# Performance work log

Measured on AMD Instinct MI355X. Metric: run time of the kernel, lower is better.

## Reference

```python
import jax, jax.numpy as jnp
import numpy as np

EMBED_DIM = 256
NUM_HEADS = 8
HEAD_DIM = EMBED_DIM // NUM_HEADS
SPARSITY_RATIO = 0.1
NEG_INF = float('-inf')


def setup_inputs() -> dict:
    key = jax.random.key(0)
    ks = jax.random.split(key, 6)
    B, S, E = 4, 2048, EMBED_DIM
    scale = 1.0 / np.sqrt(E)
    x = jax.random.normal(ks[0], (B, S, E), dtype=jnp.float32)
    Wq = jax.random.normal(ks[1], (E, E), dtype=jnp.float32) * scale
    Wk = jax.random.normal(ks[2], (E, E), dtype=jnp.float32) * scale
    Wv = jax.random.normal(ks[3], (E, E), dtype=jnp.float32) * scale
    Wo = jax.random.normal(ks[4], (E, E), dtype=jnp.float32) * scale
    z = jnp.zeros((E,), dtype=jnp.float32)
    return {"x": x, "Wq": Wq, "bq": z, "Wk": Wk, "bk": z,
            "Wv": Wv, "bv": z, "Wo": Wo, "bo": z}


def _sparse_mask(x):
    # no_grad block in torch -> stop_gradient here
    B, S, E = x.shape
    scores = jnp.einsum('bse,bte->bst', x, x) / np.sqrt(EMBED_DIM)  # [B,S,S]
    k = max(1, int(S * SPARSITY_RATIO))
    _, idx = jax.lax.top_k(scores, k)  # [B,S,k]
    sparse = jnp.zeros_like(scores)
    bi = jnp.arange(B)[:, None, None]
    si = jnp.arange(S)[None, :, None]
    sparse = sparse.at[bi, si, idx].set(1.0)
    attn_mask = jnp.where(sparse > 0, 0.0, NEG_INF).astype(x.dtype)  # [B,S,S]
    return jax.lax.stop_gradient(attn_mask)


def reference(x, Wq, bq, Wk, bk, Wv, bv, Wo, bo):
    B, S, E = x.shape
    H, D = NUM_HEADS, HEAD_DIM
    attn_mask = _sparse_mask(x)  # [B,S,S], additive 0/-inf

    q = (x @ Wq.T + bq).reshape(B, S, H, D)
    k = (x @ Wk.T + bk).reshape(B, S, H, D)
    v = (x @ Wv.T + bv).reshape(B, S, H, D)

    logits = jnp.einsum('bshd,bthd->bhst', q, k) / np.sqrt(D)  # [B,H,S,S]
    logits = logits + attn_mask[:, None, :, :]
    probs = jax.nn.softmax(logits, axis=-1)  # dropout is identity in eval

    ctx = jnp.einsum('bhst,bthd->bshd', probs, v).reshape(B, S, E)
    out = ctx @ Wo.T + bo
    attn_weights = probs.mean(axis=1)  # averaged over heads [B,S,S]
    return out, attn_weights
```

## Files before the change

kernel.cpp:

```cpp
#include <hip/hip_runtime.h>

#define SEQ  2048
#define EMB  256
#define NH   8
#define HD   32
#define NB   4
#define KTOP 204
#define IDXP 208
#define KPW  52
#define MBOUND 4e-4f

typedef unsigned long long ull;
typedef unsigned short u16;

using frag8  = __attribute__((ext_vector_type(8))) short;
using f32x4v = __attribute__((ext_vector_type(4))) float;
typedef _Float16 f16;
typedef _Float16 f16x2 __attribute__((ext_vector_type(2)));

union U4 { uint4 u; f16x2 h[4]; };
union HU { f16 h; u16 u; };

#if defined(__has_builtin)
#if __has_builtin(__builtin_amdgcn_fdot2)
#define FDOT2(a,b,c) __builtin_amdgcn_fdot2(a, b, c, false)
#endif
#endif
#ifndef FDOT2
__device__ __forceinline__ float fdot2_sw(f16x2 a, f16x2 b, float c) {
  return c + (float)a[0]*(float)b[0] + (float)a[1]*(float)b[1];
}
#define FDOT2(a,b,c) fdot2_sw(a,b,c)
#endif

__device__ __forceinline__ unsigned f2ord(float f) {
  unsigned u = __float_as_uint(f);
  return (u & 0x80000000u) ? ~u : (u | 0x80000000u);
}
__device__ __forceinline__ float ord2f(unsigned o) {
  unsigned u = (o & 0x80000000u) ? (o ^ 0x80000000u) : ~o;
  return __uint_as_float(u);
}
__device__ __forceinline__ u16 f2bf(float f) {
  unsigned u = __float_as_uint(f);
  u += 0x7FFF + ((u >> 16) & 1);
  return (u16)(u >> 16);
}
__device__ __forceinline__ float bf2f(u16 h) {
  return __uint_as_float((unsigned)h << 16);
}

__device__ __forceinline__ void tk_radix(
    const unsigned key[8], int tid, int (*hist)[256], int* sel,
    unsigned& V, int& MEQ)
{
  const int lane = tid & 63, wid = tid >> 6;
  unsigned prefix = 0;
  int k = KTOP;
#pragma unroll
  for (int p = 0; p < 4; ++p) {
    const int shift = 24 - 8 * p;
    hist[0][tid] = 0; hist[1][tid] = 0; hist[2][tid] = 0; hist[3][tid] = 0;
    __syncthreads();
#pragma unroll
    for (int j = 0; j < 8; ++j) {
      unsigned kj = key[j];
      bool ok = (p == 0) || ((kj >> (shift + 8)) == prefix);
      if (ok) atomicAdd(&hist[wid][(kj >> shift) & 255], 1);
    }
    __syncthreads();
    {
      int c = hist[0][tid] + hist[1][tid] + hist[2][tid] + hist[3][tid];
      hist[0][tid] = c;
    }
    __syncthreads();
    if (wid == 0) {
      int m0 = hist[0][lane * 4 + 0], m1 = hist[0][lane * 4 + 1];
      int m2 = hist[0][lane * 4 + 2], m3 = hist[0][lane * 4 + 3];
      int sl = m0 + m1 + m2 + m3;
      int suf = sl;
#pragma unroll
      for (int off = 1; off < 64; off <<= 1) {
        int y = __shfl_down(suf, off, 64);
        if (lane + off < 64) suf += y;
      }
      int above = suf - sl;
      if (above < k && k <= suf) {
        int bin, nk;
        if (k <= above + m3)                { bin = lane*4+3; nk = k - above; }
        else if (k <= above + m3 + m2)      { bin = lane*4+2; nk = k - above - m3; }
        else if (k <= above + m3 + m2 + m1) { bin = lane*4+1; nk = k - above - m3 - m2; }
        else                                { bin = lane*4+0; nk = k - above - m3 - m2 - m1; }
        sel[0] = bin; sel[1] = nk;
      }
    }
    __syncthreads();
    prefix = (prefix << 8) | (unsigned)sel[0];
    k = sel[1];
    __syncthreads();
  }
  V = prefix;
  MEQ = k;
}

__device__ __forceinline__ int tk_scan_excl(int v, int tid, int* wsum) {
  const int lane = tid & 63, wid = tid >> 6;
  int x = v;
#pragma unroll
  for (int off = 1; off < 64; off <<= 1) {
    int y = __shfl_up(x, off, 64);
    if (lane >= off) x += y;
  }
  if (lane == 63) wsum[wid] = x;
  __syncthreads();
  int base = 0;
  for (int w = 0; w < wid; ++w) base += wsum[w];
  return base + x - v;
}

__device__ __forceinline__ void tk_write(const unsigned key[8], unsigned V, int MEQ,
                                         int tid, u16* orow, int* wsum) {
  int ceq = 0;
#pragma unroll
  for (int j = 0; j < 8; ++j) ceq += (key[j] == V) ? 1 : 0;
  int run = tk_scan_excl(ceq, tid, wsum);
  unsigned bits = 0;
#pragma unroll
  for (int j = 0; j < 8; ++j) {
    bool e = (key[j] == V);
    bool s = (key[j] > V) || (e && (run < MEQ));
    if (e) run++;
    if (s) bits |= (1u << j);
  }
  int csel = __popc(bits);
  __syncthreads();
  int base = tk_scan_excl(csel, tid, wsum);
#pragma unroll
  for (int j = 0; j < 8; ++j)
    if ((bits >> j) & 1u) orow[base++] = (u16)(tid * 8 + j);
}

__global__ __launch_bounds__(256) void pack_x(
    const float* __restrict__ x, u16* __restrict__ xh, u16* __restrict__ xl,
    int* __restrict__ flagcnt)
{
  if (flagcnt && blockIdx.x == 0 && threadIdx.x < NB) flagcnt[threadIdx.x] = 0;
  const int i = (blockIdx.x * 256 + threadIdx.x) * 8;
  float4 a = *(const float4*)(x + i);
  float4 b = *(const float4*)(x + i + 4);
  float v[8] = {a.x,a.y,a.z,a.w,b.x,b.y,b.z,b.w};
  u16 h[8], l[8];
#pragma unroll
  for (int j = 0; j < 8; ++j) {
    h[j] = f2bf(v[j]);
    l[j] = f2bf(v[j] - bf2f(h[j]));
  }
  uint4 ph, pl;
  ph.x = h[0] | ((unsigned)h[1] << 16); ph.y = h[2] | ((unsigned)h[3] << 16);
  ph.z = h[4] | ((unsigned)h[5] << 16); ph.w = h[6] | ((unsigned)h[7] << 16);
  pl.x = l[0] | ((unsigned)l[1] << 16); pl.y = l[2] | ((unsigned)l[3] << 16);
  pl.z = l[4] | ((unsigned)l[5] << 16); pl.w = l[6] | ((unsigned)l[7] << 16);
  *(uint4*)(xh + i) = ph;
  *(uint4*)(xl + i) = pl;
}

__global__ __launch_bounds__(256) void pack_w(
    const float* __restrict__ W0, const float* __restrict__ W1,
    const float* __restrict__ W2, const float* __restrict__ W3,
    u16* __restrict__ wpk)
{
  const int m = blockIdx.y;
  const float* W = (m == 0) ? W0 : (m == 1) ? W1 : (m == 2) ? W2 : W3;
  const int i = (blockIdx.x * 256 + threadIdx.x) * 8;
  float4 a = *(const float4*)(W + i);
  float4 b = *(const float4*)(W + i + 4);
  float v[8] = {a.x,a.y,a.z,a.w,b.x,b.y,b.z,b.w};
  u16 h[8], l[8];
#pragma unroll
  for (int j = 0; j < 8; ++j) {
    h[j] = f2bf(v[j]);
    l[j] = f2bf(v[j] - bf2f(h[j]));
  }
  uint4 ph, pl;
  ph.x = h[0] | ((unsigned)h[1] << 16); ph.y = h[2] | ((unsigned)h[3] << 16);
  ph.z = h[4] | ((unsigned)h[5] << 16); ph.w = h[6] | ((unsigned)h[7] << 16);
  pl.x = l[0] | ((unsigned)l[1] << 16); pl.y = l[2] | ((unsigned)l[3] << 16);
  pl.z = l[4] | ((unsigned)l[5] << 16); pl.w = l[6] | ((unsigned)l[7] << 16);
  u16* dh = wpk + (size_t)m * 2 * 65536;
  *(uint4*)(dh + i) = ph;
  *(uint4*)(dh + 65536 + i) = pl;
}

__global__ __launch_bounds__(256) void scores_mfma(
    const u16* __restrict__ xh, const u16* __restrict__ xl,
    float* __restrict__ C)
{
  __shared__ u16 Ah[128 * 40], Al[128 * 40], Bh[128 * 40], Bl[128 * 40];
  const int tid = threadIdx.x;
  const int m0 = blockIdx.x * 128, n0 = blockIdx.y * 128;
  const u16* xhB = xh + (size_t)blockIdx.z * SEQ * EMB;
  const u16* xlB = xl + (size_t)blockIdx.z * SEQ * EMB;
  float* Cb = C + (size_t)blockIdx.z * SEQ * SEQ;
  const int wv = tid >> 6, ln = tid & 63;
  const int quad = ln >> 4, r16 = ln & 15;
  const int wm = (wv & 1) * 64, wn = (wv >> 1) * 64;
  const int srow = tid >> 1, shalf = (tid & 1) * 16;

  f32x4v acc[4][4];
#pragma unroll
  for (int i = 0; i < 4; ++i)
#pragma unroll
    for (int j = 0; j < 4; ++j) acc[i][j] = (f32x4v){0.f, 0.f, 0.f, 0.f};

  for (int k0 = 0; k0 < EMB; k0 += 32) {
    __syncthreads();
    {
      size_t ga = (size_t)(m0 + srow) * EMB + k0 + shalf;
      size_t gb = (size_t)(n0 + srow) * EMB + k0 + shalf;
      uint4 ah0 = *(const uint4*)(xhB + ga), ah1 = *(const uint4*)(xhB + ga + 8);
      uint4 al0 = *(const uint4*)(xlB + ga), al1 = *(const uint4*)(xlB + ga + 8);
      uint4 bh0 = *(const uint4*)(xhB + gb), bh1 = *(const uint4*)(xhB + gb + 8);
      uint4 bl0 = *(const uint4*)(xlB + gb), bl1 = *(const uint4*)(xlB + gb + 8);
      int o = srow * 40 + shalf;
      *(uint4*)&Ah[o] = ah0; *(uint4*)&Ah[o + 8] = ah1;
      *(uint4*)&Al[o] = al0; *(uint4*)&Al[o + 8] = al1;
      *(uint4*)&Bh[o] = bh0; *(uint4*)&Bh[o + 8] = bh1;
      *(uint4*)&Bl[o] = bl0; *(uint4*)&Bl[o + 8] = bl1;
    }
    __syncthreads();
    frag8 fbh[4], fbl[4];
#pragma unroll
    for (int nt = 0; nt < 4; ++nt) {
      int ob = (wn + nt * 16 + r16) * 40 + quad * 8;
      fbh[nt] = *(const frag8*)&Bh[ob];
      fbl[nt] = *(const frag8*)&Bl[ob];
    }
#pragma unroll
    for (int mt = 0; mt < 4; ++mt) {
      int oa = (wm + mt * 16 + r16) * 40 + quad * 8;
      frag8 fah = *(const frag8*)&Ah[oa];
      frag8 fal = *(const frag8*)&Al[oa];
#pragma unroll
      for (int nt = 0; nt < 4; ++nt) {
        acc[mt][nt] = __builtin_amdgcn_mfma_f32_16x16x32_bf16(fah, fbh[nt], acc[mt][nt], 0, 0, 0);
        acc[mt][nt] = __builtin_amdgcn_mfma_f32_16x16x32_bf16(fah, fbl[nt], acc[mt][nt], 0, 0, 0);
        acc[mt][nt] = __builtin_amdgcn_mfma_f32_16x16x32_bf16(fal, fbh[nt], acc[mt][nt], 0, 0, 0);
        acc[mt][nt] = __builtin_amdgcn_mfma_f32_16x16x32_bf16(fal, fbl[nt], acc[mt][nt], 0, 0, 0);
      }
    }
  }
#pragma unroll
  for (int mt = 0; mt < 4; ++mt)
#pragma unroll
    for (int nt = 0; nt < 4; ++nt) {
      int cg = n0 + wn + nt * 16 + r16;
      int rb = m0 + wm + mt * 16 + quad * 4;
#pragma unroll
      for (int r = 0; r < 4; ++r)
        Cb[(size_t)(rb + r) * SEQ + cg] = acc[mt][nt][r] * 0.0625f;
    }
}

__global__ __launch_bounds__(256) void qkv_mfma(
    const u16* __restrict__ xh, const u16* __restrict__ xl,
    const u16* __restrict__ wpk,
    const float* __restrict__ bq, const float* __restrict__ bk,
    const float* __restrict__ bv,
    u16* __restrict__ qo, u16* __restrict__ ko, u16* __restrict__ vo)
{
  const int z = blockIdx.z;
  const u16* Wh = wpk + (size_t)z * 2 * 65536;
  const u16* Wl = Wh + 65536;
  const float* bias = (z == 0) ? bq : (z == 1) ? bk : bv;
  u16* out = (z == 0) ? qo : (z == 1) ? ko : vo;

  __shared__ u16 Ah[128 * 40], Al[128 * 40], Bh[128 * 40], Bl[128 * 40];
  const int tid = threadIdx.x;
  const int m0 = blockIdx.x * 128, n0 = blockIdx.y * 128;
  const int wv = tid >> 6, ln = tid & 63;
  const int quad = ln >> 4, r16 = ln & 15;
  const int wm = (wv & 1) * 64, wn = (wv >> 1) * 64;
  const int srow = tid >> 1, shalf = (tid & 1) * 16;

  f32x4v acc[4][4];
#pragma unroll
  for (int i = 0; i < 4; ++i)
#pragma unroll
    for (int j = 0; j < 4; ++j) acc[i][j] = (f32x4v){0.f, 0.f, 0.f, 0.f};

  for (int k0 = 0; k0 < EMB; k0 += 32) {
    __syncthreads();
    {
      size_t ga = (size_t)(m0 + srow) * EMB + k0 + shalf;
      size_t gb = (size_t)(n0 + srow) * EMB + k0 + shalf;
      uint4 ah0 = *(const uint4*)(xh + ga), ah1 = *(const uint4*)(xh + ga + 8);
      uint4 al0 = *(const uint4*)(xl + ga), al1 = *(const uint4*)(xl + ga + 8);
      uint4 bh0 = *(const uint4*)(Wh + gb), bh1 = *(const uint4*)(Wh + gb + 8);
      uint4 bl0 = *(const uint4*)(Wl + gb), bl1 = *(const uint4*)(Wl + gb + 8);
      int o = srow * 40 + shalf;
      *(uint4*)&Ah[o] = ah0; *(uint4*)&Ah[o + 8] = ah1;
      *(uint4*)&Al[o] = al0; *(uint4*)&Al[o + 8] = al1;
      *(uint4*)&Bh[o] = bh0; *(uint4*)&Bh[o + 8] = bh1;
      *(uint4*)&Bl[o] = bl0; *(uint4*)&Bl[o + 8] = bl1;
    }
    __syncthreads();
    frag8 fbh[4], fbl[4];
#pragma unroll
    for (int nt = 0; nt < 4; ++nt) {
      int ob = (wn + nt * 16 + r16) * 40 + quad * 8;
      fbh[nt] = *(const frag8*)&Bh[ob];
      fbl[nt] = *(const frag8*)&Bl[ob];
    }
#pragma unroll
    for (int mt = 0; mt < 4; ++mt) {
      int oa = (wm + mt * 16 + r16) * 40 + quad * 8;
      frag8 fah = *(const frag8*)&Ah[oa];
      frag8 fal = *(const frag8*)&Al[oa];
#pragma unroll
      for (int nt = 0; nt < 4; ++nt) {
        acc[mt][nt] = __builtin_amdgcn_mfma_f32_16x16x32_bf16(fah, fbh[nt], acc[mt][nt], 0, 0, 0);
        acc[mt][nt] = __builtin_amdgcn_mfma_f32_16x16x32_bf16(fah, fbl[nt], acc[mt][nt], 0, 0, 0);
        acc[mt][nt] = __builtin_amdgcn_mfma_f32_16x16x32_bf16(fal, fbh[nt], acc[mt][nt], 0, 0, 0);
      }
    }
  }
#pragma unroll
  for (int nt = 0; nt < 4; ++nt) {
    int cg = n0 + wn + nt * 16 + r16;
    float bvv = bias[cg];
#pragma unroll
    for (int mt = 0; mt < 4; ++mt) {
      int rb = m0 + wm + mt * 16 + quad * 4;
#pragma unroll
      for (int r = 0; r < 4; ++r) {
        HU hu; hu.h = (f16)(acc[mt][nt][r] + bvv);
        out[(size_t)(rb + r) * EMB + cg] = hu.u;
      }
    }
  }
}

__global__ __launch_bounds__(256) void out_mfma(
    const u16* __restrict__ ch, const u16* __restrict__ cl,
    const u16* __restrict__ wpk, const float* __restrict__ bias,
    float* __restrict__ out)
{
  const u16* Wh = wpk + (size_t)3 * 2 * 65536;
  const u16* Wl = Wh + 65536;
  __shared__ u16 Ah[128 * 40], Al[128 * 40], Bh[128 * 40], Bl[128 * 40];
  const int tid = threadIdx.x;
  const int m0 = blockIdx.x * 128, n0 = blockIdx.y * 128;
  const int wv = tid >> 6, ln = tid & 63;
  const int quad = ln >> 4, r16 = ln & 15;
  const int wm = (wv & 1) * 64, wn = (wv >> 1) * 64;
  const int srow = tid >> 1, shalf = (tid & 1) * 16;

  f32x4v acc[4][4];
#pragma unroll
  for (int i = 0; i < 4; ++i)
#pragma unroll
    for (int j = 0; j < 4; ++j) acc[i][j] = (f32x4v){0.f, 0.f, 0.f, 0.f};

  for (int k0 = 0; k0 < EMB; k0 += 32) {
    __syncthreads();
    {
      size_t ga = (size_t)(m0 + srow) * EMB + k0 + shalf;
      size_t gb = (size_t)(n0 + srow) * EMB + k0 + shalf;
      uint4 ah0 = *(const uint4*)(ch + ga), ah1 = *(const uint4*)(ch + ga + 8);
      uint4 al0 = *(const uint4*)(cl + ga), al1 = *(const uint4*)(cl + ga + 8);
      uint4 bh0 = *(const uint4*)(Wh + gb), bh1 = *(const uint4*)(Wh + gb + 8);
      uint4 bl0 = *(const uint4*)(Wl + gb), bl1 = *(const uint4*)(Wl + gb + 8);
      int o = srow * 40 + shalf;
      *(uint4*)&Ah[o] = ah0; *(uint4*)&Ah[o + 8] = ah1;
      *(uint4*)&Al[o] = al0; *(uint4*)&Al[o + 8] = al1;
      *(uint4*)&Bh[o] = bh0; *(uint4*)&Bh[o + 8] = bh1;
      *(uint4*)&Bl[o] = bl0; *(uint4*)&Bl[o + 8] = bl1;
    }
    __syncthreads();
    frag8 fbh[4], fbl[4];
#pragma unroll
    for (int nt = 0; nt < 4; ++nt) {
      int ob = (wn + nt * 16 + r16) * 40 + quad * 8;
      fbh[nt] = *(const frag8*)&Bh[ob];
      fbl[nt] = *(const frag8*)&Bl[ob];
    }
#pragma unroll
    for (int mt = 0; mt < 4; ++mt) {
      int oa = (wm + mt * 16 + r16) * 40 + quad * 8;
      frag8 fah = *(const frag8*)&Ah[oa];
      frag8 fal = *(const frag8*)&Al[oa];
#pragma unroll
      for (int nt = 0; nt < 4; ++nt) {
        acc[mt][nt] = __builtin_amdgcn_mfma_f32_16x16x32_bf16(fah, fbh[nt], acc[mt][nt], 0, 0, 0);
        acc[mt][nt] = __builtin_amdgcn_mfma_f32_16x16x32_bf16(fah, fbl[nt], acc[mt][nt], 0, 0, 0);
        acc[mt][nt] = __builtin_amdgcn_mfma_f32_16x16x32_bf16(fal, fbh[nt], acc[mt][nt], 0, 0, 0);
      }
    }
  }
#pragma unroll
  for (int nt = 0; nt < 4; ++nt) {
    int cg = n0 + wn + nt * 16 + r16;
    float bvv = bias[cg];
#pragma unroll
    for (int mt = 0; mt < 4; ++mt) {
      int rb = m0 + wm + mt * 16 + quad * 4;
#pragma unroll
      for (int r = 0; r < 4; ++r)
        out[(size_t)(rb + r) * EMB + cg] = acc[mt][nt][r] + bvv;
    }
  }
}

__global__ __launch_bounds__(256) void topk_idx(
    const float* __restrict__ scores, u16* __restrict__ idxl,
    int* __restrict__ flagcnt, int* __restrict__ flaglist)
{
  __shared__ int hist[4][256];
  __shared__ int sel[2];
  __shared__ int wsum[4];
  __shared__ unsigned wmax[4];
  const int r = blockIdx.x;
  const int tid = threadIdx.x;
  const int lane = tid & 63, wid = tid >> 6;
  const float* row = scores + (size_t)r * SEQ;
  unsigned key[8];
  {
    float4 f0 = *(const float4*)(row + tid * 8);
    float4 f1 = *(const float4*)(row + tid * 8 + 4);
    key[0]=f2ord(f0.x); key[1]=f2ord(f0.y); key[2]=f2ord(f0.z); key[3]=f2ord(f0.w);
    key[4]=f2ord(f1.x); key[5]=f2ord(f1.y); key[6]=f2ord(f1.z); key[7]=f2ord(f1.w);
  }
  unsigned V; int MEQ;
  tk_radix(key, tid, hist, sel, V, MEQ);

  {
    int ceq = 0; unsigned mk = 0;
#pragma unroll
    for (int j = 0; j < 8; ++j) {
      ceq += (key[j] == V) ? 1 : 0;
      if (key[j] < V && key[j] > mk) mk = key[j];
    }
#pragma unroll
    for (int off = 32; off > 0; off >>= 1) {
      ceq += __shfl_down(ceq, off, 64);
      unsigned o = (unsigned)__shfl_down((int)mk, off, 64);
      if (o > mk) mk = o;
    }
    if (lane == 0) { wsum[wid] = ceq; wmax[wid] = mk; }
    __syncthreads();
    if (tid == 0) {
      int EQ = wsum[0] + wsum[1] + wsum[2] + wsum[3];
      unsigned m2 = wmax[0];
      for (int w = 1; w < 4; ++w) if (wmax[w] > m2) m2 = wmax[w];
      bool flag = (EQ > MEQ) || !(ord2f(V) - ord2f(m2) >= MBOUND);
      if (flag) {
        int bb = r >> 11;
        int p = atomicAdd(&flagcnt[bb], 1);
        flaglist[bb * SEQ + p] = r & (SEQ - 1);
      }
    }
    __syncthreads();
  }

  tk_write(key, V, MEQ, tid, idxl + (size_t)r * IDXP, wsum);
}

__global__ __launch_bounds__(256) void fixup_gemm(
    const float* __restrict__ x, const int* __restrict__ flagcnt,
    const int* __restrict__ flaglist, float* __restrict__ attn)
{
  const int b = blockIdx.z;
  const int n = flagcnt[b];
  const int g0 = blockIdx.y * 64;
  if (g0 >= n) return;
  __shared__ float As[16][68];
  __shared__ float Bs[16][68];
  __shared__ int rowsh[64];
  const int tid = threadIdx.x;
  const int n0 = blockIdx.x * 64;
  if (tid < 64) {
    int gi = g0 + tid;
    rowsh[tid] = (gi < n) ? flaglist[b * SEQ + gi] : -1;
  }
  __syncthreads();
  const float* xb = x + (size_t)b * SEQ * EMB;
  const int lm = tid >> 2;
  const int lk = (tid & 3) << 2;
  const int mt = tid >> 4;
  const int nt = tid & 15;
  const int arow = rowsh[lm];
  const int arowL = (arow < 0) ? 0 : arow;
  float acc[4][4] = {{0.f}};
  for (int k0 = 0; k0 < EMB; k0 += 16) {
    float4 av = *(const float4*)(xb + (size_t)arowL * EMB + k0 + lk);
    float4 bv = *(const float4*)(xb + (size_t)(n0 + lm) * EMB + k0 + lk);
    __syncthreads();
    As[lk+0][lm] = av.x; As[lk+1][lm] = av.y; As[lk+2][lm] = av.z; As[lk+3][lm] = av.w;
    Bs[lk+0][lm] = bv.x; Bs[lk+1][lm] = bv.y; Bs[lk+2][lm] = bv.z; Bs[lk+3][lm] = bv.w;
    __syncthreads();
#pragma unroll
    for (int kk = 0; kk < 16; ++kk) {
      float4 a4 = *(const float4*)&As[kk][mt << 2];
      float4 b4 = *(const float4*)&Bs[kk][nt << 2];
      acc[0][0] += a4.x*b4.x; acc[0][1] += a4.x*b4.y; acc[0][2] += a4.x*b4.z; acc[0][3] += a4.x*b4.w;
      acc[1][0] += a4.y*b4.x; acc[1][1] += a4.y*b4.y; acc[1][2] += a4.y*b4.z; acc[1][3] += a4.y*b4.w;
      acc[2][0] += a4.z*b4.x; acc[2][1] += a4.z*b4.y; acc[2][2] += a4.z*b4.z; acc[2][3] += a4.z*b4.w;
      acc[3][0] += a4.w*b4.x; acc[3][1] += a4.w*b4.y; acc[3][2] += a4.w*b4.z; acc[3][3] += a4.w*b4.w;
    }
  }
  float* attnB = attn + (size_t)b * SEQ * SEQ;
#pragma unroll
  for (int r = 0; r < 4; ++r) {
    int rr = rowsh[(mt << 2) + r];
    if (rr >= 0) {
      float4 o;
      o.x = acc[r][0] * 0.0625f; o.y = acc[r][1] * 0.0625f;
      o.z = acc[r][2] * 0.0625f; o.w = acc[r][3] * 0.0625f;
      *(float4*)(attnB + (size_t)rr * SEQ + n0 + (nt << 2)) = o;
    }
  }
}

__global__ __launch_bounds__(256) void topk_fixup(
    const float* __restrict__ attn, const int* __restrict__ flagcnt,
    const int* __restrict__ flaglist, u16* __restrict__ idxl)
{
  const int b = blockIdx.y;
  if ((int)blockIdx.x >= flagcnt[b]) return;
  const int r = b * SEQ + flaglist[b * SEQ + blockIdx.x];
  __shared__ int hist[4][256];
  __shared__ int sel[2];
  __shared__ int wsum[4];
  const int tid = threadIdx.x;
  const float* row = attn + (size_t)r * SEQ;
  unsigned key[8];
  {
    float4 f0 = *(const float4*)(row + tid * 8);
    float4 f1 = *(const float4*)(row + tid * 8 + 4);
    key[0]=f2ord(f0.x); key[1]=f2ord(f0.y); key[2]=f2ord(f0.z); key[3]=f2ord(f0.w);
    key[4]=f2ord(f1.x); key[5]=f2ord(f1.y); key[6]=f2ord(f1.z); key[7]=f2ord(f1.w);
  }
  unsigned V; int MEQ;
  tk_radix(key, tid, hist, sel, V, MEQ);
  tk_write(key, V, MEQ, tid, idxl + (size_t)r * IDXP, wsum);
}

__global__ __launch_bounds__(256) void sparse_attn(
    const u16* __restrict__ qf, const u16* __restrict__ kf,
    const u16* __restrict__ vf, const u16* __restrict__ idxl,
    float* __restrict__ attn, float* __restrict__ ctxb)
{
  const int lin = blockIdx.x;
  const int b = lin & 3;
  const int q = (lin >> 3) + (((lin >> 2) & 1) << 10);
  const int tid = threadIdx.x;
  const int wv = tid >> 6, ln = tid & 63;
  const int half = ln >> 5, sl = ln & 31;
  const int h = sl >> 2, d0 = sl * 8;
  const int lb = sl * 16;
  __shared__ int   ish[IDXP];
  __shared__ int   koff[IDXP];
  __shared__ float psh[IDXP * 9 + 4];
  __shared__ float idsh[NH];
  __shared__ float csh[8][264];
  __shared__ float rsh[SEQ];

  const int row = b * SEQ + q;
  if (tid < KTOP) {
    int idx = (int)idxl[(size_t)row * IDXP + tid];
    ish[tid] = idx;
    koff[tid] = idx << 9;
  } else if (tid < IDXP) {
    ish[tid] = 0; koff[tid] = 0;
  }
  if (tid < 32) psh[(KTOP + (tid >> 3)) * 9 + (tid & 7)] = 0.f;

  float4 z4 = make_float4(0.f, 0.f, 0.f, 0.f);
  *(float4*)&rsh[tid * 4]        = z4;
  *(float4*)&rsh[1024 + tid * 4] = z4;

  U4 qv;
  qv.u = *(const uint4*)((const char*)(qf + (size_t)row * EMB) + lb);

  __syncthreads();

  const float scale = 0.17677669529663687f;
  const char* kbC = (const char*)(kf + (size_t)(b * SEQ) * EMB);
  const int jb = wv * KPW;
#pragma unroll 4
  for (int t = 0; t < KPW; t += 2) {
    const int j = jb + t + half;
    U4 kv;
    kv.u = *(const uint4*)(kbC + (koff[j] + lb));
    float s = FDOT2(qv.h[0], kv.h[0],
              FDOT2(qv.h[1], kv.h[1],
              FDOT2(qv.h[2], kv.h[2],
              FDOT2(qv.h[3], kv.h[3], 0.f))));
    s += __shfl_xor(s, 1, 64);
    s += __shfl_xor(s, 2, 64);
    if ((sl & 3) == 0 && j < KTOP) psh[j * 9 + h] = __expf(s * scale);
  }
  __syncthreads();

  {
    int h2 = tid >> 5, l = tid & 31;
    float sden = 0.f;
    for (int j = l; j < KTOP; j += 32) sden += psh[j * 9 + h2];
#pragma unroll
    for (int off = 16; off > 0; off >>= 1) sden += __shfl_down(sden, off, 32);
    if (l == 0) idsh[h2] = 1.0f / sden;
  }
  __syncthreads();

  if (tid < KTOP) {
    float ps = 0.f;
#pragma unroll
    for (int hh = 0; hh < 8; ++hh) {
      float pp = psh[tid * 9 + hh] * idsh[hh];
      psh[tid * 9 + hh] = pp;
      ps += pp;
    }
    rsh[ish[tid]] = ps * 0.125f;
  }
  __syncthreads();

  {
    float* arow = attn + (size_t)row * SEQ;
    *(float4*)(arow + tid * 4)        = *(const float4*)&rsh[tid * 4];
    *(float4*)(arow + 1024 + tid * 4) = *(const float4*)&rsh[1024 + tid * 4];
  }

  {
    const char* vbC = (const char*)(vf + (size_t)(b * SEQ) * EMB);
    float a8[8] = {0.f,0.f,0.f,0.f,0.f,0.f,0.f,0.f};
#pragma unroll 4
    for (int t = 0; t < KPW; t += 2) {
      const int j = jb + t + half;
      float p = psh[j * 9 + h];
      U4 vv;
      vv.u = *(const uint4*)(vbC + (koff[j] + lb));
      a8[0] += p * (float)vv.h[0][0]; a8[1] += p * (float)vv.h[0][1];
      a8[2] += p * (float)vv.h[1][0]; a8[3] += p * (float)vv.h[1][1];
      a8[4] += p * (float)vv.h[2][0]; a8[5] += p * (float)vv.h[2][1];
      a8[6] += p * (float)vv.h[3][0]; a8[7] += p * (float)vv.h[3][1];
    }
    const int pi = wv * 2 + half;
    *(float4*)&csh[pi][d0]     = make_float4(a8[0], a8[1], a8[2], a8[3]);
    *(float4*)&csh[pi][d0 + 4] = make_float4(a8[4], a8[5], a8[6], a8[7]);
  }
  __syncthreads();
  if (tid < 64) {
    float4 o = z4;
#pragma unroll
    for (int g = 0; g < 8; ++g) {
      float4 v = *(const float4*)&csh[g][tid * 4];
      o.x += v.x; o.y += v.y; o.z += v.z; o.w += v.w;
    }
    *(float4*)(ctxb + (size_t)row * EMB + tid * 4) = o;
  }
}

extern "C" void kernel_launch(void* const* d_in, const int* in_sizes, int n_in,
                              void* d_out, int out_size, void* d_ws, size_t ws_size,
                              hipStream_t stream)
{
  const float* x  = (const float*)d_in[0];
  const float* Wq = (const float*)d_in[1];
  const float* bq = (const float*)d_in[2];
  const float* Wk = (const float*)d_in[3];
  const float* bk = (const float*)d_in[4];
  const float* Wv = (const float*)d_in[5];
  const float* bv = (const float*)d_in[6];
  const float* Wo = (const float*)d_in[7];
  const float* bo = (const float*)d_in[8];

  float* out  = (float*)d_out;
  float* attn = out + (size_t)NB * SEQ * EMB;

  const size_t NSE = (size_t)NB * SEQ * EMB;
  u16* xh  = (u16*)d_ws;
  u16* xl  = xh + NSE;
  u16* qf  = xl + NSE;
  u16* kf  = qf + NSE;
  u16* vf  = kf + NSE;
  u16* wpk = vf + NSE;
  float* ctxb = (float*)(wpk + 4 * 2 * 65536);
  u16* idxl = (u16*)(ctxb + NSE);
  int* flagcnt  = (int*)(idxl + (size_t)NB * SEQ * IDXP);
  int* flaglist = flagcnt + NB;

  const dim3 blk(256);

  pack_x<<<dim3(1024), blk, 0, stream>>>(x, xh, xl, flagcnt);
  pack_w<<<dim3(32, 4), blk, 0, stream>>>(Wq, Wk, Wv, Wo, wpk);

  qkv_mfma<<<dim3(64, 2, 3), blk, 0, stream>>>(xh, xl, wpk, bq, bk, bv, qf, kf, vf);

  scores_mfma<<<dim3(16, 16, NB), blk, 0, stream>>>(xh, xl, attn);

  topk_idx<<<dim3(NB * SEQ), blk, 0, stream>>>(attn, idxl, flagcnt, flaglist);
  fixup_gemm<<<dim3(32, 32, NB), blk, 0, stream>>>(x, flagcnt, flaglist, attn);
  topk_fixup<<<dim3(SEQ, NB), blk, 0, stream>>>(attn, flagcnt, flaglist, idxl);

  sparse_attn<<<dim3(SEQ * NB), blk, 0, stream>>>(qf, kf, vf, idxl, attn, ctxb);

  pack_x<<<dim3(1024), blk, 0, stream>>>(ctxb, xh, xl, nullptr);
  out_mfma<<<dim3(64, 2), blk, 0, stream>>>(xh, xl, wpk, bo, out);
}
```

Before: 347.6 us.

## Merge pack kernels and GEMM launches; fold ctx split into output GEMM

```diff
diff --git a/kernel.cpp b/kernel.cpp
--- a/kernel.cpp
+++ b/kernel.cpp
@@ -140,14 +140,30 @@
     if ((bits >> j) & 1u) orow[base++] = (u16)(tid * 8 + j);
 }
 
-__global__ __launch_bounds__(256) void pack_x(
-    const float* __restrict__ x, u16* __restrict__ xh, u16* __restrict__ xl,
+__global__ __launch_bounds__(256) void pack_all(
+    const float* __restrict__ x,
+    const float* __restrict__ W0, const float* __restrict__ W1,
+    const float* __restrict__ W2, const float* __restrict__ W3,
+    u16* __restrict__ xh, u16* __restrict__ xl, u16* __restrict__ wpk,
     int* __restrict__ flagcnt)
 {
-  if (flagcnt && blockIdx.x == 0 && threadIdx.x < NB) flagcnt[threadIdx.x] = 0;
-  const int i = (blockIdx.x * 256 + threadIdx.x) * 8;
-  float4 a = *(const float4*)(x + i);
-  float4 b = *(const float4*)(x + i + 4);
+  const int lin = blockIdx.x;
+  if (lin == 0 && threadIdx.x < NB) flagcnt[threadIdx.x] = 0;
+  const float* src; u16 *dh, *dl; int i;
+  if (lin < 1024) {
+    src = x;
+    i = (lin * 256 + threadIdx.x) * 8;
+    dh = xh; dl = xl;
+  } else {
+    int j = lin - 1024;
+    int m = j >> 5, bx = j & 31;
+    src = (m == 0) ? W0 : (m == 1) ? W1 : (m == 2) ? W2 : W3;
+    i = (bx * 256 + threadIdx.x) * 8;
+    dh = wpk + (size_t)m * 2 * 65536;
+    dl = dh + 65536;
+  }
+  float4 a = *(const float4*)(src + i);
+  float4 b = *(const float4*)(src + i + 4);
   float v[8] = {a.x,a.y,a.z,a.w,b.x,b.y,b.z,b.w};
   u16 h[8], l[8];
 #pragma unroll
@@ -160,47 +176,21 @@
   ph.z = h[4] | ((unsigned)h[5] << 16); ph.w = h[6] | ((unsigned)h[7] << 16);
   pl.x = l[0] | ((unsigned)l[1] << 16); pl.y = l[2] | ((unsigned)l[3] << 16);
   pl.z = l[4] | ((unsigned)l[5] << 16); pl.w = l[6] | ((unsigned)l[7] << 16);
-  *(uint4*)(xh + i) = ph;
-  *(uint4*)(xl + i) = pl;
-}
-
-__global__ __launch_bounds__(256) void pack_w(
-    const float* __restrict__ W0, const float* __restrict__ W1,
-    const float* __restrict__ W2, const float* __restrict__ W3,
-    u16* __restrict__ wpk)
-{
-  const int m = blockIdx.y;
-  const float* W = (m == 0) ? W0 : (m == 1) ? W1 : (m == 2) ? W2 : W3;
-  const int i = (blockIdx.x * 256 + threadIdx.x) * 8;
-  float4 a = *(const float4*)(W + i);
-  float4 b = *(const float4*)(W + i + 4);
-  float v[8] = {a.x,a.y,a.z,a.w,b.x,b.y,b.z,b.w};
-  u16 h[8], l[8];
-#pragma unroll
-  for (int j = 0; j < 8; ++j) {
-    h[j] = f2bf(v[j]);
-    l[j] = f2bf(v[j] - bf2f(h[j]));
-  }
-  uint4 ph, pl;
-  ph.x = h[0] | ((unsigned)h[1] << 16); ph.y = h[2] | ((unsigned)h[3] << 16);
-  ph.z = h[4] | ((unsigned)h[5] << 16); ph.w = h[6] | ((unsigned)h[7] << 16);
-  pl.x = l[0] | ((unsigned)l[1] << 16); pl.y = l[2] | ((unsigned)l[3] << 16);
-  pl.z = l[4] | ((unsigned)l[5] << 16); pl.w = l[6] | ((unsigned)l[7] << 16);
-  u16* dh = wpk + (size_t)m * 2 * 65536;
   *(uint4*)(dh + i) = ph;
-  *(uint4*)(dh + 65536 + i) = pl;
-}
-
-__global__ __launch_bounds__(256) void scores_mfma(
+  *(uint4*)(dl + i) = pl;
+}
+
+__global__ __launch_bounds__(256) void fused_gemms(
     const u16* __restrict__ xh, const u16* __restrict__ xl,
-    float* __restrict__ C)
+    const u16* __restrict__ wpk,
+    const float* __restrict__ bq, const float* __restrict__ bk,
+    const float* __restrict__ bv,
+    u16* __restrict__ qo, u16* __restrict__ ko, u16* __restrict__ vo,
+    float* __restrict__ attnC)
 {
   __shared__ u16 Ah[128 * 40], Al[128 * 40], Bh[128 * 40], Bl[128 * 40];
+  const int lin = blockIdx.x;
   const int tid = threadIdx.x;
-  const int m0 = blockIdx.x * 128, n0 = blockIdx.y * 128;
-  const u16* xhB = xh + (size_t)blockIdx.z * SEQ * EMB;
-  const u16* xlB = xl + (size_t)blockIdx.z * SEQ * EMB;
-  float* Cb = C + (size_t)blockIdx.z * SEQ * SEQ;
   const int wv = tid >> 6, ln = tid & 63;
   const int quad = ln >> 4, r16 = ln & 15;
   const int wm = (wv & 1) * 64, wn = (wv >> 1) * 64;
@@ -212,138 +202,123 @@
 #pragma unroll
     for (int j = 0; j < 4; ++j) acc[i][j] = (f32x4v){0.f, 0.f, 0.f, 0.f};
 
-  for (int k0 = 0; k0 < EMB; k0 += 32) {
-    __syncthreads();
-    {
-      size_t ga = (size_t)(m0 + srow) * EMB + k0 + shalf;
-      size_t gb = (size_t)(n0 + srow) * EMB + k0 + shalf;
-      uint4 ah0 = *(const uint4*)(xhB + ga), ah1 = *(const uint4*)(xhB + ga + 8);
-      uint4 al0 = *(const uint4*)(xlB + ga), al1 = *(const uint4*)(xlB + ga + 8);
-      uint4 bh0 = *(const uint4*)(xhB + gb), bh1 = *(const uint4*)(xhB + gb + 8);
-      uint4 bl0 = *(const uint4*)(xlB + gb), bl1 = *(const uint4*)(xlB + gb + 8);
-      int o = srow * 40 + shalf;
-      *(uint4*)&Ah[o] = ah0; *(uint4*)&Ah[o + 8] = ah1;
-      *(uint4*)&Al[o] = al0; *(uint4*)&Al[o + 8] = al1;
-      *(uint4*)&Bh[o] = bh0; *(uint4*)&Bh[o + 8] = bh1;
-      *(uint4*)&Bl[o] = bl0; *(uint4*)&Bl[o + 8] = bl1;
-    }
-    __syncthreads();
-    frag8 fbh[4], fbl[4];
-#pragma unroll
-    for (int nt = 0; nt < 4; ++nt) {
-      int ob = (wn + nt * 16 + r16) * 40 + quad * 8;
-      fbh[nt] = *(const frag8*)&Bh[ob];
-      fbl[nt] = *(const frag8*)&Bl[ob];
-    }
-#pragma unroll
-    for (int mt = 0; mt < 4; ++mt) {
-      int oa = (wm + mt * 16 + r16) * 40 + quad * 8;
-      frag8 fah = *(const frag8*)&Ah[oa];
-      frag8 fal = *(const frag8*)&Al[oa];
+  if (lin < 1024) {
+    const int m0 = (lin & 15) * 128, n0 = ((lin >> 4) & 15) * 128;
+    const int b = lin >> 8;
+    const u16* xhB = xh + (size_t)b * SEQ * EMB;
+    const u16* xlB = xl + (size_t)b * SEQ * EMB;
+    float* Cb = attnC + (size_t)b * SEQ * SEQ;
+    for (int k0 = 0; k0 < EMB; k0 += 32) {
+      __syncthreads();
+      {
+        size_t ga = (size_t)(m0 + srow) * EMB + k0 + shalf;
+        size_t gb = (size_t)(n0 + srow) * EMB + k0 + shalf;
+        uint4 ah0 = *(const uint4*)(xhB + ga), ah1 = *(const uint4*)(xhB + ga + 8);
+        uint4 al0 = *(const uint4*)(xlB + ga), al1 = *(const uint4*)(xlB + ga + 8);
+        uint4 bh0 = *(const uint4*)(xhB + gb), bh1 = *(const uint4*)(xhB + gb + 8);
+        uint4 bl0 = *(const uint4*)(xlB + gb), bl1 = *(const uint4*)(xlB + gb + 8);
+        int o = srow * 40 + shalf;
+        *(uint4*)&Ah[o] = ah0; *(uint4*)&Ah[o + 8] = ah1;
+        *(uint4*)&Al[o] = al0; *(uint4*)&Al[o + 8] = al1;
+        *(uint4*)&Bh[o] = bh0; *(uint4*)&Bh[o + 8] = bh1;
+        *(uint4*)&Bl[o] = bl0; *(uint4*)&Bl[o + 8] = bl1;
+      }
+      __syncthreads();
+      frag8 fbh[4], fbl[4];
 #pragma unroll
       for (int nt = 0; nt < 4; ++nt) {
-        acc[mt][nt] = __builtin_amdgcn_mfma_f32_16x16x32_bf16(fah, fbh[nt], acc[mt][nt], 0, 0, 0);
-        acc[mt][nt] = __builtin_amdgcn_mfma_f32_16x16x32_bf16(fah, fbl[nt], acc[mt][nt], 0, 0, 0);
-        acc[mt][nt] = __builtin_amdgcn_mfma_f32_16x16x32_bf16(fal, fbh[nt], acc[mt][nt], 0, 0, 0);
-        acc[mt][nt] = __builtin_amdgcn_mfma_f32_16x16x32_bf16(fal, fbl[nt], acc[mt][nt], 0, 0, 0);
-      }
-    }
-  }
-#pragma unroll
-  for (int mt = 0; mt < 4; ++mt)
+        int ob = (wn + nt * 16 + r16) * 40 + quad * 8;
+        fbh[nt] = *(const frag8*)&Bh[ob];
+        fbl[nt] = *(const frag8*)&Bl[ob];
+      }
+#pragma unroll
+      for (int mt = 0; mt < 4; ++mt) {
+        int oa = (wm + mt * 16 + r16) * 40 + quad * 8;
+        frag8 fah = *(const frag8*)&Ah[oa];
+        frag8 fal = *(const frag8*)&Al[oa];
+#pragma unroll
+        for (int nt = 0; nt < 4; ++nt) {
+          acc[mt][nt] = __builtin_amdgcn_mfma_f32_16x16x32_bf16(fah, fbh[nt], acc[mt][nt], 0, 0, 0);
+          acc[mt][nt] = __builtin_amdgcn_mfma_f32_16x16x32_bf16(fah, fbl[nt], acc[mt][nt], 0, 0, 0);
+          acc[mt][nt] = __builtin_amdgcn_mfma_f32_16x16x32_bf16(fal, fbh[nt], acc[mt][nt], 0, 0, 0);
+          acc[mt][nt] = __builtin_amdgcn_mfma_f32_16x16x32_bf16(fal, fbl[nt], acc[mt][nt], 0, 0, 0);
+        }
+      }
+    }
+#pragma unroll
+    for (int mt = 0; mt < 4; ++mt)
+#pragma unroll
+      for (int nt = 0; nt < 4; ++nt) {
+        int cg = n0 + wn + nt * 16 + r16;
+        int rb = m0 + wm + mt * 16 + quad * 4;
+#pragma unroll
+        for (int r = 0; r < 4; ++r)
+          Cb[(size_t)(rb + r) * SEQ + cg] = acc[mt][nt][r] * 0.0625f;
+      }
+  } else {
+    const int j = lin - 1024;
+    const int m0 = (j & 63) * 128, n0 = ((j >> 6) & 1) * 128;
+    const int z = j >> 7;
+    const u16* Wh = wpk + (size_t)z * 2 * 65536;
+    const u16* Wl = Wh + 65536;
+    const float* bias = (z == 0) ? bq : (z == 1) ? bk : bv;
+    u16* out = (z == 0) ? qo : (z == 1) ? ko : vo;
+    for (int k0 = 0; k0 < EMB; k0 += 32) {
+      __syncthreads();
+      {
+        size_t ga = (size_t)(m0 + srow) * EMB + k0 + shalf;
+        size_t gb = (size_t)(n0 + srow) * EMB + k0 + shalf;
+        uint4 ah0 = *(const uint4*)(xh + ga), ah1 = *(const uint4*)(xh + ga + 8);
+        uint4 al0 = *(const uint4*)(xl + ga), al1 = *(const uint4*)(xl + ga + 8);
+        uint4 bh0 = *(const uint4*)(Wh + gb), bh1 = *(const uint4*)(Wh + gb + 8);
+        uint4 bl0 = *(const uint4*)(Wl + gb), bl1 = *(const uint4*)(Wl + gb + 8);
+        int o = srow * 40 + shalf;
+        *(uint4*)&Ah[o] = ah0; *(uint4*)&Ah[o + 8] = ah1;
+        *(uint4*)&Al[o] = al0; *(uint4*)&Al[o + 8] = al1;
+        *(uint4*)&Bh[o] = bh0; *(uint4*)&Bh[o + 8] = bh1;
+        *(uint4*)&Bl[o] = bl0; *(uint4*)&Bl[o + 8] = bl1;
+      }
+      __syncthreads();
+      frag8 fbh[4], fbl[4];
+#pragma unroll
+      for (int nt = 0; nt < 4; ++nt) {
+        int ob = (wn + nt * 16 + r16) * 40 + quad * 8;
+        fbh[nt] = *(const frag8*)&Bh[ob];
+        fbl[nt] = *(const frag8*)&Bl[ob];
+      }
+#pragma unroll
+      for (int mt = 0; mt < 4; ++mt) {
+        int oa = (wm + mt * 16 + r16) * 40 + quad * 8;
+        frag8 fah = *(const frag8*)&Ah[oa];
+        frag8 fal = *(const frag8*)&Al[oa];
+#pragma unroll
+        for (int nt = 0; nt < 4; ++nt) {
+          acc[mt][nt] = __builtin_amdgcn_mfma_f32_16x16x32_bf16(fah, fbh[nt], acc[mt][nt], 0, 0, 0);
+          acc[mt][nt] = __builtin_amdgcn_mfma_f32_16x16x32_bf16(fah, fbl[nt], acc[mt][nt], 0, 0, 0);
+          acc[mt][nt] = __builtin_amdgcn_mfma_f32_16x16x32_bf16(fal, fbh[nt], acc[mt][nt], 0, 0, 0);
+        }
+      }
+    }
 #pragma unroll
     for (int nt = 0; nt < 4; ++nt) {
       int cg = n0 + wn + nt * 16 + r16;
-      int rb = m0 + wm + mt * 16 + quad * 4;
-#pragma unroll
-      for (int r = 0; r < 4; ++r)
-        Cb[(size_t)(rb + r) * SEQ + cg] = acc[mt][nt][r] * 0.0625f;
-    }
-}
-
-__global__ __launch_bounds__(256) void qkv_mfma(
-    const u16* __restrict__ xh, const u16* __restrict__ xl,
-    const u16* __restrict__ wpk,
-    const float* __restrict__ bq, const float* __restrict__ bk,
-    const float* __restrict__ bv,
-    u16* __restrict__ qo, u16* __restrict__ ko, u16* __restrict__ vo)
-{
-  const int z = blockIdx.z;
-  const u16* Wh = wpk + (size_t)z * 2 * 65536;
-  const u16* Wl = Wh + 65536;
-  const float* bias = (z == 0) ? bq : (z == 1) ? bk : bv;
-  u16* out = (z == 0) ? qo : (z == 1) ? ko : vo;
-
-  __shared__ u16 Ah[128 * 40], Al[128 * 40], Bh[128 * 40], Bl[128 * 40];
-  const int tid = threadIdx.x;
-  const int m0 = blockIdx.x * 128, n0 = blockIdx.y * 128;
-  const int wv = tid >> 6, ln = tid & 63;
-  const int quad = ln >> 4, r16 = ln & 15;
-  const int wm = (wv & 1) * 64, wn = (wv >> 1) * 64;
-  const int srow = tid >> 1, shalf = (tid & 1) * 16;
-
-  f32x4v acc[4][4];
-#pragma unroll
-  for (int i = 0; i < 4; ++i)
-#pragma unroll
-    for (int j = 0; j < 4; ++j) acc[i][j] = (f32x4v){0.f, 0.f, 0.f, 0.f};
-
-  for (int k0 = 0; k0 < EMB; k0 += 32) {
-    __syncthreads();
-    {
-      size_t ga = (size_t)(m0 + srow) * EMB + k0 + shalf;
-      size_t gb = (size_t)(n0 + srow) * EMB + k0 + shalf;
-      uint4 ah0 = *(const uint4*)(xh + ga), ah1 = *(const uint4*)(xh + ga + 8);
-      uint4 al0 = *(const uint4*)(xl + ga), al1 = *(const uint4*)(xl + ga + 8);
-      uint4 bh0 = *(const uint4*)(Wh + gb), bh1 = *(const uint4*)(Wh + gb + 8);
-      uint4 bl0 = *(const uint4*)(Wl + gb), bl1 = *(const uint4*)(Wl + gb + 8);
-      int o = srow * 40 + shalf;
-      *(uint4*)&Ah[o] = ah0; *(uint4*)&Ah[o + 8] = ah1;
-      *(uint4*)&Al[o] = al0; *(uint4*)&Al[o + 8] = al1;
-      *(uint4*)&Bh[o] = bh0; *(uint4*)&Bh[o + 8] = bh1;
-      *(uint4*)&Bl[o] = bl0; *(uint4*)&Bl[o + 8] = bl1;
-    }
-    __syncthreads();
-    frag8 fbh[4], fbl[4];
-#pragma unroll
-    for (int nt = 0; nt < 4; ++nt) {
-      int ob = (wn + nt * 16 + r16) * 40 + quad * 8;
-      fbh[nt] = *(const frag8*)&Bh[ob];
-      fbl[nt] = *(const frag8*)&Bl[ob];
-    }
-#pragma unroll
-    for (int mt = 0; mt < 4; ++mt) {
-      int oa = (wm + mt * 16 + r16) * 40 + quad * 8;
-      frag8 fah = *(const frag8*)&Ah[oa];
-      frag8 fal = *(const frag8*)&Al[oa];
-#pragma unroll
-      for (int nt = 0; nt < 4; ++nt) {
-        acc[mt][nt] = __builtin_amdgcn_mfma_f32_16x16x32_bf16(fah, fbh[nt], acc[mt][nt], 0, 0, 0);
-        acc[mt][nt] = __builtin_amdgcn_mfma_f32_16x16x32_bf16(fah, fbl[nt], acc[mt][nt], 0, 0, 0);
-        acc[mt][nt] = __builtin_amdgcn_mfma_f32_16x16x32_bf16(fal, fbh[nt], acc[mt][nt], 0, 0, 0);
-      }
-    }
-  }
-#pragma unroll
-  for (int nt = 0; nt < 4; ++nt) {
-    int cg = n0 + wn + nt * 16 + r16;
-    float bvv = bias[cg];
-#pragma unroll
-    for (int mt = 0; mt < 4; ++mt) {
-      int rb = m0 + wm + mt * 16 + quad * 4;
-#pragma unroll
-      for (int r = 0; r < 4; ++r) {
-        HU hu; hu.h = (f16)(acc[mt][nt][r] + bvv);
-        out[(size_t)(rb + r) * EMB + cg] = hu.u;
+      float bvv = bias[cg];
+#pragma unroll
+      for (int mt = 0; mt < 4; ++mt) {
+        int rb = m0 + wm + mt * 16 + quad * 4;
+#pragma unroll
+        for (int r = 0; r < 4; ++r) {
+          HU hu; hu.h = (f16)(acc[mt][nt][r] + bvv);
+          out[(size_t)(rb + r) * EMB + cg] = hu.u;
+        }
       }
     }
   }
 }
 
 __global__ __launch_bounds__(256) void out_mfma(
-    const u16* __restrict__ ch, const u16* __restrict__ cl,
-    const u16* __restrict__ wpk, const float* __restrict__ bias,
-    float* __restrict__ out)
+    const float* __restrict__ ctx, const u16* __restrict__ wpk,
+    const float* __restrict__ bias, float* __restrict__ out)
 {
   const u16* Wh = wpk + (size_t)3 * 2 * 65536;
   const u16* Wl = Wh + 65536;
@@ -365,14 +340,36 @@
     __syncthreads();
     {
       size_t ga = (size_t)(m0 + srow) * EMB + k0 + shalf;
+      float4 c0 = *(const float4*)(ctx + ga);
+      float4 c1 = *(const float4*)(ctx + ga + 4);
+      float4 c2 = *(const float4*)(ctx + ga + 8);
+      float4 c3 = *(const float4*)(ctx + ga + 12);
+      float v[16] = {c0.x,c0.y,c0.z,c0.w, c1.x,c1.y,c1.z,c1.w,
+                     c2.x,c2.y,c2.z,c2.w, c3.x,c3.y,c3.z,c3.w};
+      u16 hh[16], ll[16];
+#pragma unroll
+      for (int jj = 0; jj < 16; ++jj) {
+        hh[jj] = f2bf(v[jj]);
+        ll[jj] = f2bf(v[jj] - bf2f(hh[jj]));
+      }
+      int o = srow * 40 + shalf;
+#pragma unroll
+      for (int g = 0; g < 2; ++g) {
+        uint4 ph, pl;
+        ph.x = hh[g*8+0] | ((unsigned)hh[g*8+1] << 16);
+        ph.y = hh[g*8+2] | ((unsigned)hh[g*8+3] << 16);
+        ph.z = hh[g*8+4] | ((unsigned)hh[g*8+5] << 16);
+        ph.w = hh[g*8+6] | ((unsigned)hh[g*8+7] << 16);
+        pl.x = ll[g*8+0] | ((unsigned)ll[g*8+1] << 16);
+        pl.y = ll[g*8+2] | ((unsigned)ll[g*8+3] << 16);
+        pl.z = ll[g*8+4] | ((unsigned)ll[g*8+5] << 16);
+        pl.w = ll[g*8+6] | ((unsigned)ll[g*8+7] << 16);
+        *(uint4*)&Ah[o + g*8] = ph;
+        *(uint4*)&Al[o + g*8] = pl;
+      }
       size_t gb = (size_t)(n0 + srow) * EMB + k0 + shalf;
-      uint4 ah0 = *(const uint4*)(ch + ga), ah1 = *(const uint4*)(ch + ga + 8);
-      uint4 al0 = *(const uint4*)(cl + ga), al1 = *(const uint4*)(cl + ga + 8);
       uint4 bh0 = *(const uint4*)(Wh + gb), bh1 = *(const uint4*)(Wh + gb + 8);
       uint4 bl0 = *(const uint4*)(Wl + gb), bl1 = *(const uint4*)(Wl + gb + 8);
-      int o = srow * 40 + shalf;
-      *(uint4*)&Ah[o] = ah0; *(uint4*)&Ah[o + 8] = ah1;
-      *(uint4*)&Al[o] = al0; *(uint4*)&Al[o + 8] = al1;
       *(uint4*)&Bh[o] = bh0; *(uint4*)&Bh[o + 8] = bh1;
       *(uint4*)&Bl[o] = bl0; *(uint4*)&Bl[o + 8] = bl1;
     }
@@ -562,8 +559,8 @@
   __shared__ int   koff[IDXP];
   __shared__ float psh[IDXP * 9 + 4];
   __shared__ float idsh[NH];
-  __shared__ float csh[8][264];
-  __shared__ float rsh[SEQ];
+  __shared__ float rcsh[2112];
+#define CSH(i, j) rcsh[(i) * 264 + (j)]
 
   const int row = b * SEQ + q;
   if (tid < KTOP) {
@@ -576,8 +573,8 @@
   if (tid < 32) psh[(KTOP + (tid >> 3)) * 9 + (tid & 7)] = 0.f;
 
   float4 z4 = make_float4(0.f, 0.f, 0.f, 0.f);
-  *(float4*)&rsh[tid * 4]        = z4;
-  *(float4*)&rsh[1024 + tid * 4] = z4;
+  *(float4*)&rcsh[tid * 4]        = z4;
+  *(float4*)&rcsh[1024 + tid * 4] = z4;
 
   U4 qv;
   qv.u = *(const uint4*)((const char*)(qf + (size_t)row * EMB) + lb);
@@ -620,15 +617,16 @@
       psh[tid * 9 + hh] = pp;
       ps += pp;
     }
-    rsh[ish[tid]] = ps * 0.125f;
+    rcsh[ish[tid]] = ps * 0.125f;
   }
   __syncthreads();
 
   {
     float* arow = attn + (size_t)row * SEQ;
-    *(float4*)(arow + tid * 4)        = *(const float4*)&rsh[tid * 4];
-    *(float4*)(arow + 1024 + tid * 4) = *(const float4*)&rsh[1024 + tid * 4];
-  }
+    *(float4*)(arow + tid * 4)        = *(const float4*)&rcsh[tid * 4];
+    *(float4*)(arow + 1024 + tid * 4) = *(const float4*)&rcsh[1024 + tid * 4];
+  }
+  __syncthreads();
 
   {
     const char* vbC = (const char*)(vf + (size_t)(b * SEQ) * EMB);
@@ -645,19 +643,20 @@
       a8[6] += p * (float)vv.h[3][0]; a8[7] += p * (float)vv.h[3][1];
     }
     const int pi = wv * 2 + half;
-    *(float4*)&csh[pi][d0]     = make_float4(a8[0], a8[1], a8[2], a8[3]);
-    *(float4*)&csh[pi][d0 + 4] = make_float4(a8[4], a8[5], a8[6], a8[7]);
+    *(float4*)&CSH(pi, d0)     = make_float4(a8[0], a8[1], a8[2], a8[3]);
+    *(float4*)&CSH(pi, d0 + 4) = make_float4(a8[4], a8[5], a8[6], a8[7]);
   }
   __syncthreads();
   if (tid < 64) {
     float4 o = z4;
 #pragma unroll
     for (int g = 0; g < 8; ++g) {
-      float4 v = *(const float4*)&csh[g][tid * 4];
+      float4 v = *(const float4*)&CSH(g, tid * 4);
       o.x += v.x; o.y += v.y; o.z += v.z; o.w += v.w;
     }
     *(float4*)(ctxb + (size_t)row * EMB + tid * 4) = o;
   }
+#undef CSH
 }
 
 extern "C" void kernel_launch(void* const* d_in, const int* in_sizes, int n_in,
@@ -691,12 +690,10 @@
 
   const dim3 blk(256);
 
-  pack_x<<<dim3(1024), blk, 0, stream>>>(x, xh, xl, flagcnt);
-  pack_w<<<dim3(32, 4), blk, 0, stream>>>(Wq, Wk, Wv, Wo, wpk);
-
-  qkv_mfma<<<dim3(64, 2, 3), blk, 0, stream>>>(xh, xl, wpk, bq, bk, bv, qf, kf, vf);
-
-  scores_mfma<<<dim3(16, 16, NB), blk, 0, stream>>>(xh, xl, attn);
+  pack_all<<<dim3(1152), blk, 0, stream>>>(x, Wq, Wk, Wv, Wo, xh, xl, wpk, flagcnt);
+
+  fused_gemms<<<dim3(1408), blk, 0, stream>>>(xh, xl, wpk, bq, bk, bv,
+                                              qf, kf, vf, attn);
 
   topk_idx<<<dim3(NB * SEQ), blk, 0, stream>>>(attn, idxl, flagcnt, flaglist);
   fixup_gemm<<<dim3(32, 32, NB), blk, 0, stream>>>(x, flagcnt, flaglist, attn);
@@ -704,6 +701,5 @@
 
   sparse_attn<<<dim3(SEQ * NB), blk, 0, stream>>>(qf, kf, vf, idxl, attn, ctxb);
 
-  pack_x<<<dim3(1024), blk, 0, stream>>>(ctxb, xh, xl, nullptr);
-  out_mfma<<<dim3(64, 2), blk, 0, stream>>>(xh, xl, wpk, bo, out);
-}
+  out_mfma<<<dim3(64, 2), blk, 0, stream>>>(ctxb, wpk, bo, out);
+}
```

Result: faster. 323.3 us (-7.0%).
